# Kernel tuning notes

Measured on AMD Instinct MI355X. Metric: run time of the kernel, lower is better.

Reference implementation:

```python
import jax, jax.numpy as jnp
import numpy as np
from jax import lax

DIM = 512
MED = 2 * DIM            # expansion_ratio * dim
NF = 4                   # num_filters
SIZE = 64                # spatial size (H = W = size)
FS = SIZE // 2 + 1       # rfft filter size
HR = int(0.5 * DIM)      # reweight hidden (NNConv, 1x1 convs)
HS = int(0.5 * DIM)      # spatial_reweight hidden (Convs, 3x3 convs)
B = 16


def _conv1x1(x, w, b):
    # x: [B,C,H,W], w: [O,C,1,1]
    return jnp.einsum('bchw,oc->bohw', x, w[:, :, 0, 0]) + b[None, :, None, None]


def _conv3x3(x, w, b):
    # x: [B,C,H,W], w: [O,C,3,3], padding=1
    return lax.conv_general_dilated(x, w, (1, 1), 'SAME') + b[None, :, None, None]


def setup_inputs() -> dict:
    key = jax.random.key(0)
    ks = jax.random.split(key, 12)
    n = lambda k, shape, s=0.02: jax.random.normal(k, shape, jnp.float32) * s
    return dict(
        x=jax.random.normal(ks[0], (B, DIM, SIZE, SIZE), jnp.float32),
        w_pw1=n(ks[1], (MED, DIM)),                 # pwconv1 (Linear, no bias)
        w_pw2=n(ks[2], (DIM, MED)),                 # pwconv2 (Linear, no bias)
        star_scale=jnp.ones((1,), jnp.float32),     # StarReLU scale
        star_bias=jnp.zeros((1,), jnp.float32),     # StarReLU bias
        rw_fc1_w=n(ks[3], (HR, DIM, 1, 1)), rw_fc1_b=jnp.zeros((HR,), jnp.float32),
        rw_conv_w=n(ks[4], (HR, HR, 1, 1)), rw_conv_b=jnp.zeros((HR,), jnp.float32),
        rw_fc2_w=n(ks[5], (NF * MED, HR, 1, 1)), rw_fc2_b=jnp.zeros((NF * MED,), jnp.float32),
        sp_fc1_w=n(ks[6], (HS, DIM, 3, 3)), sp_fc1_b=jnp.zeros((HS,), jnp.float32),
        sp_fc2_w=n(ks[7], (NF * MED, HS, 3, 3)), sp_fc2_b=jnp.zeros((NF * MED,), jnp.float32),
        complex_weights=n(ks[8], (SIZE, FS, NF, 2), 0.02),
        spatial_weights=n(ks[9], (SIZE, SIZE, NF), 0.03),
    )


def reference(x, w_pw1, w_pw2, star_scale, star_bias,
              rw_fc1_w, rw_fc1_b, rw_conv_w, rw_conv_b, rw_fc2_w, rw_fc2_b,
              sp_fc1_w, sp_fc1_b, sp_fc2_w, sp_fc2_b,
              complex_weights, spatial_weights):
    Bn, _, H, W = x.shape
    # --- routing branch (NNConv: 1x1 conv -> relu -> 1x1 conv -> relu -> 1x1 conv) ---
    r = jax.nn.relu(_conv1x1(x, rw_fc1_w, rw_fc1_b))
    r = jax.nn.relu(_conv1x1(r, rw_conv_w, rw_conv_b))
    r = _conv1x1(r, rw_fc2_w, rw_fc2_b)                      # [B, NF*MED, H, W]
    routeing = jax.nn.softmax(r.mean(axis=(2, 3)).reshape(Bn, NF, MED), axis=1)
    # --- spatial routing branch (Convs: 3x3 conv -> relu -> 3x3 conv) ---
    s = jax.nn.relu(_conv3x3(x, sp_fc1_w, sp_fc1_b))
    s = _conv3x3(s, sp_fc2_w, sp_fc2_b)                      # [B, NF*MED, H, W]
    spatial_routeing = jax.nn.softmax(s.mean(axis=(2, 3)).reshape(Bn, NF, MED), axis=1)
    # --- main path ---
    xc = jnp.transpose(x, (0, 2, 3, 1))                      # [B,H,W,DIM]
    xp = jnp.einsum('bhwc,mc->bhwm', xc, w_pw1)              # pwconv1 -> [B,H,W,MED]
    xp = star_scale * jnp.square(jax.nn.relu(xp)) + star_bias  # StarReLU
    xf = jnp.fft.rfft2(xp, axes=(1, 2), norm='ortho')        # [B,H,FS,MED] complex64
    cw = lax.complex(complex_weights[..., 0], complex_weights[..., 1])  # [H,FS,NF]
    weight = jnp.einsum('bfc,hwf->bhwc', routeing.astype(cw.dtype), cw)  # [B,H,FS,MED]
    spatial_weight = jnp.einsum('bfc,hwf->bhwc', spatial_routeing, spatial_weights)  # [B,H,W,MED]
    xs = jnp.fft.irfft2(xf * weight, s=(H, W), axes=(1, 2), norm='ortho')
    out = xp * spatial_weight + xs                            # spatial gating + FFT filter
    out = jnp.einsum('bhwm,dm->bhwd', out, w_pw2)             # pwconv2
    return jnp.transpose(out, (0, 3, 1, 2))                   # [B,DIM,H,W]
```

## Files before the change

### kernel.cpp

```cpp
#include <hip/hip_runtime.h>

#define HW    4096
#define DIMC  512
#define MEDC  1024
#define HRC   256
#define HSC   256
#define NBATCH 16

typedef __attribute__((ext_vector_type(8))) short bf16x8;
typedef __attribute__((ext_vector_type(4))) float f32x4;

static const size_t R1_OFF    = 0;
static const size_t XT_OFF    = 8388608;
static const size_t WCONV_OFF = 25165824;
static const size_t WR1_OFF   = 25755648;
static const size_t WRC_OFF   = 25821184;
static const size_t XP_OFF    = 0;
static const size_t WB1_OFF   = 67108864;
static const size_t WB2_OFF   = 67371008;
static const size_t MEAN_OFF  = 67633152;
static const size_t AGG_OFF   = MEAN_OFF + 4096;
static const size_t TAP_OFF   = AGG_OFF + 36864;
static const size_t ROUTE_OFF = TAP_OFF + 36864;
static const size_t SR_OFF    = ROUTE_OFF + 65536;
static const size_t WS_END    = SR_OFF + 65536;

__device__ __forceinline__ unsigned short f2bf(float f) {
  unsigned u = __float_as_uint(f);
  unsigned r = (u + 0x7fffu + ((u >> 16) & 1u)) >> 16;
  return (unsigned short)r;
}

__global__ __launch_bounds__(256) void cvt_bf16(
    const float* __restrict__ src, unsigned short* __restrict__ dst, int n)
{
  int i = blockIdx.x * 256 + threadIdx.x;
  if (i < n) dst[i] = f2bf(src[i]);
}

__global__ __launch_bounds__(256) void xpose_bf16(
    const float* __restrict__ x, unsigned short* __restrict__ xT)
{
  __shared__ unsigned short T[32][33];
  const int tid = threadIdx.x;
  const int p0 = blockIdx.x * 32, c0 = blockIdx.y * 32, bb = blockIdx.z;
#pragma unroll
  for (int i = 0; i < 4; i++) {
    int idx = i * 256 + tid;
    int c_l = idx >> 5, p_l = idx & 31;
    T[c_l][p_l] = f2bf(x[((size_t)(bb * DIMC + c0 + c_l)) * HW + p0 + p_l]);
  }
  __syncthreads();
#pragma unroll
  for (int i = 0; i < 4; i++) {
    int idx = i * 256 + tid;
    int p_l = idx >> 5, c_l = idx & 31;
    xT[((size_t)bb * HW + p0 + p_l) * DIMC + c0 + c_l] = T[c_l][p_l];
  }
}

__global__ __launch_bounds__(256) void wconv_bf16(
    const float* __restrict__ w, unsigned short* __restrict__ wbf)
{
  int idx = blockIdx.x * 256 + threadIdx.x;
  if (idx < HSC * DIMC) {
#pragma unroll
    for (int t = 0; t < 9; t++)
      wbf[(size_t)t * (HSC * DIMC) + idx] = f2bf(w[(size_t)idx * 9 + t]);
  }
}

template<int EPI, int ASRC>
__global__ __launch_bounds__(256) void gemm_bf16(
    const void* __restrict__ Aptr, const unsigned short* __restrict__ Wb,
    const float* __restrict__ bias, float* __restrict__ Cf,
    unsigned short* __restrict__ Cb, float* __restrict__ meansum,
    const float* __restrict__ star_scale, const float* __restrict__ star_bias,
    int K, int Ntot)
{
  __shared__ __align__(16) unsigned short As[128 * 40];
  __shared__ __align__(16) unsigned short Bs[128 * 40];
  const int tid = threadIdx.x;
  const int pix0 = blockIdx.x * 128;
  const int n0g = blockIdx.y * 128;
  const int bb = blockIdx.z;
  const int wid = tid >> 6, lane = tid & 63;
  const int lo = lane & 15, hi = lane >> 4;
  const int wm = wid >> 1, wn = wid & 1;

  f32x4 acc[4][4];
#pragma unroll
  for (int mi = 0; mi < 4; mi++)
#pragma unroll
    for (int ni = 0; ni < 4; ni++) acc[mi][ni] = (f32x4){0.f, 0.f, 0.f, 0.f};

  const int nsteps = K >> 5;
  for (int s = 0; s < nsteps; s++) {
    const int c0 = s * 32;
    if (ASRC == 0) {
      const unsigned short* AT = (const unsigned short*)Aptr;
#pragma unroll
      for (int it = 0; it < 2; it++) {
        int idx = it * 256 + tid;
        int p = idx >> 2, co = (idx & 3) * 8;
        uint4 v = *(const uint4*)&AT[((size_t)bb * HW + pix0 + p) * K + c0 + co];
        *(uint4*)&As[p * 40 + co] = v;
      }
    } else {
      const float* Af = (const float*)Aptr;
#pragma unroll
      for (int it = 0; it < 16; it++) {
        int idx = it * 256 + tid;
        int k_l = idx >> 7, p_l = idx & 127;
        float v = Af[((size_t)bb * K + c0 + k_l) * HW + pix0 + p_l];
        As[p_l * 40 + k_l] = f2bf(v);
      }
    }
#pragma unroll
    for (int it = 0; it < 2; it++) {
      int idx = it * 256 + tid;
      int o = idx >> 2, co = (idx & 3) * 8;
      uint4 v = *(const uint4*)&Wb[(size_t)(n0g + o) * K + c0 + co];
      *(uint4*)&Bs[o * 40 + co] = v;
    }
    __syncthreads();

    bf16x8 a[4], bq[4];
#pragma unroll
    for (int mi = 0; mi < 4; mi++)
      a[mi] = *(const bf16x8*)&As[(wm * 64 + mi * 16 + lo) * 40 + hi * 8];
#pragma unroll
    for (int ni = 0; ni < 4; ni++)
      bq[ni] = *(const bf16x8*)&Bs[(wn * 64 + ni * 16 + lo) * 40 + hi * 8];
#pragma unroll
    for (int mi = 0; mi < 4; mi++)
#pragma unroll
      for (int ni = 0; ni < 4; ni++)
        acc[mi][ni] = __builtin_amdgcn_mfma_f32_16x16x32_bf16(a[mi], bq[ni], acc[mi][ni], 0, 0, 0);
    __syncthreads();
  }

  if (EPI == 3) {
#pragma unroll
    for (int ni = 0; ni < 4; ni++) {
      const int n = n0g + wn * 64 + ni * 16 + lo;
      const float bia = bias[n];
      float T = 0.f;
#pragma unroll
      for (int mi = 0; mi < 4; mi++)
#pragma unroll
        for (int r = 0; r < 4; r++)
          T += fmaxf(acc[mi][ni][r] + bia, 0.f);
      T += __shfl_xor(T, 16);
      T += __shfl_xor(T, 32);
      if (hi == 0) atomicAdd(&meansum[bb * Ntot + n], T);
    }
    return;
  }

  if (EPI == 1) {
#pragma unroll
    for (int ni = 0; ni < 4; ni++) {
      const int n = n0g + wn * 64 + ni * 16 + lo;
      const float bia = bias[n];
#pragma unroll
      for (int mi = 0; mi < 4; mi++)
#pragma unroll
        for (int r = 0; r < 4; r++) {
          const int pix = pix0 + wm * 64 + mi * 16 + hi * 4 + r;
          Cb[((size_t)bb * HW + pix) * Ntot + n] = f2bf(fmaxf(acc[mi][ni][r] + bia, 0.f));
        }
    }
    return;
  }

  float ss = 1.f, sb = 0.f;
  if (EPI == 2) { ss = star_scale[0]; sb = star_bias[0]; }
#pragma unroll
  for (int ni = 0; ni < 4; ni++) {
    const int n = n0g + wn * 64 + ni * 16 + lo;
#pragma unroll
    for (int mi = 0; mi < 4; mi++) {
      const int pixb = pix0 + wm * 64 + mi * 16 + hi * 4;
      float4 v;
      float* vv = (float*)&v;
#pragma unroll
      for (int r = 0; r < 4; r++) {
        float t = acc[mi][ni][r];
        if (EPI == 2) { t = fmaxf(t, 0.f); t = ss * t * t + sb; }
        vv[r] = t;
      }
      *(float4*)&Cf[((size_t)bb * Ntot + n) * HW + pixb] = v;
    }
  }
}

__global__ __launch_bounds__(256) void conv3_mfma(
    const unsigned short* __restrict__ xT, const unsigned short* __restrict__ wbf,
    const float* __restrict__ bias, float* __restrict__ agg)
{
  __shared__ __align__(16) unsigned short As[128 * 40];
  __shared__ __align__(16) unsigned short Bs[128 * 40];
  const int tid = threadIdx.x;
  const int bx = blockIdx.x;
  const int n0g = blockIdx.y * 128;
  const int bb = blockIdx.z;
  const int h0 = bx * 2;
  const int wid = tid >> 6;
  const int lane = tid & 63;
  const int lo = lane & 15, hi = lane >> 4;
  const int wm = wid >> 1;
  const int wn = wid & 1;

  f32x4 acc[4][4];
#pragma unroll
  for (int mi = 0; mi < 4; mi++)
#pragma unroll
    for (int ni = 0; ni < 4; ni++) acc[mi][ni] = (f32x4){0.f, 0.f, 0.f, 0.f};

  for (int s = 0; s < 144; s++) {
    const int t = s >> 4;
    const int c0 = (s & 15) * 32;
    const int di = t / 3 - 1, dj = t % 3 - 1;
#pragma unroll
    for (int it = 0; it < 2; it++) {
      int idx = it * 256 + tid;
      int pix = idx >> 2, co = (idx & 3) * 8;
      int h = h0 + (pix >> 6) + di;
      int col = (pix & 63) + dj;
      uint4 v = make_uint4(0u, 0u, 0u, 0u);
      if (h >= 0 && h < 64 && col >= 0 && col < 64)
        v = *(const uint4*)&xT[((size_t)bb * HW + h * 64 + col) * DIMC + c0 + co];
      *(uint4*)&As[pix * 40 + co] = v;
    }
#pragma unroll
    for (int it = 0; it < 2; it++) {
      int idx = it * 256 + tid;
      int o = idx >> 2, co = (idx & 3) * 8;
      uint4 v = *(const uint4*)&wbf[((size_t)t * (HSC * DIMC)) + (size_t)(n0g + o) * DIMC + c0 + co];
      *(uint4*)&Bs[o * 40 + co] = v;
    }
    __syncthreads();

    bf16x8 a[4], bfr[4];
#pragma unroll
    for (int mi = 0; mi < 4; mi++)
      a[mi] = *(const bf16x8*)&As[(wm * 64 + mi * 16 + lo) * 40 + hi * 8];
#pragma unroll
    for (int ni = 0; ni < 4; ni++)
      bfr[ni] = *(const bf16x8*)&Bs[(wn * 64 + ni * 16 + lo) * 40 + hi * 8];
#pragma unroll
    for (int mi = 0; mi < 4; mi++)
#pragma unroll
      for (int ni = 0; ni < 4; ni++)
        acc[mi][ni] = __builtin_amdgcn_mfma_f32_16x16x32_bf16(a[mi], bfr[ni], acc[mi][ni], 0, 0, 0);
    __syncthreads();
  }

  const int h = h0 + wm;
#pragma unroll
  for (int ni = 0; ni < 4; ni++) {
    const int o = n0g + wn * 64 + ni * 16 + lo;
    const float bia = bias[o];
    float T = 0.f;
#pragma unroll
    for (int mi = 0; mi < 4; mi++)
#pragma unroll
      for (int r = 0; r < 4; r++)
        T += fmaxf(acc[mi][ni][r] + bia, 0.f);
    T += __shfl_xor(T, 16);
    T += __shfl_xor(T, 32);
    float* ag = &agg[((size_t)bb * HSC + o) * 9];
    if (hi == 0) {
      atomicAdd(ag + 0, T);
      if (h == 0)  atomicAdd(ag + 1, T);
      if (h == 63) atomicAdd(ag + 2, T);
      float c0v = fmaxf(acc[0][ni][0] + bia, 0.f);
      atomicAdd(ag + 3, c0v);
      if (h == 0)  atomicAdd(ag + 5, c0v);
      if (h == 63) atomicAdd(ag + 7, c0v);
    }
    if (hi == 3) {
      float cwv = fmaxf(acc[3][ni][3] + bia, 0.f);
      atomicAdd(ag + 4, cwv);
      if (h == 0)  atomicAdd(ag + 6, cwv);
      if (h == 63) atomicAdd(ag + 8, cwv);
    }
  }
}

__global__ void tap_compute(const float* __restrict__ agg, float* __restrict__ tap)
{
  int b = blockIdx.x; int c = threadIdx.x;
  const float* a = &agg[((size_t)b * HSC + c) * 9];
  float T = a[0], R0 = a[1], RH = a[2], C0 = a[3], CW = a[4];
  float s00 = a[5], s0W = a[6], sH0 = a[7], sHW = a[8];
  float* tp = &tap[((size_t)b * HSC + c) * 9];
#pragma unroll
  for (int i = 0; i < 3; i++)
#pragma unroll
    for (int j = 0; j < 3; j++) {
      int di = i - 1, dj = j - 1;
      float v = T;
      if (di == -1) v -= RH; else if (di == 1) v -= R0;
      if (dj == -1) v -= CW; else if (dj == 1) v -= C0;
      if (di == -1 && dj == -1) v += sHW;
      if (di == -1 && dj ==  1) v += sH0;
      if (di ==  1 && dj == -1) v += s0W;
      if (di ==  1 && dj ==  1) v += s00;
      tp[i * 3 + j] = v * (1.f / 4096.f);
    }
}

__global__ __launch_bounds__(256) void route_softmax(
    const float* __restrict__ meansum, const float* __restrict__ W,
    const float* __restrict__ bias, float* __restrict__ route)
{
  __shared__ float mv[HRC];
  int b = blockIdx.y;
  int m = blockIdx.x * 256 + threadIdx.x;
  mv[threadIdx.x] = meansum[b * HRC + threadIdx.x] * (1.f / 4096.f);
  __syncthreads();
  float l[4];
#pragma unroll
  for (int f = 0; f < 4; f++) {
    int o = f * MEDC + m;
    float accv = bias[o];
    const float* wr = &W[(size_t)o * HRC];
    for (int c = 0; c < HRC; c++) accv += wr[c] * mv[c];
    l[f] = accv;
  }
  float mx = fmaxf(fmaxf(l[0], l[1]), fmaxf(l[2], l[3]));
  float e[4], s = 0.f;
#pragma unroll
  for (int f = 0; f < 4; f++) { e[f] = expf(l[f] - mx); s += e[f]; }
  float inv = 1.f / s;
#pragma unroll
  for (int f = 0; f < 4; f++) route[((size_t)b * 4 + f) * MEDC + m] = e[f] * inv;
}

__global__ __launch_bounds__(256) void sproute_softmax(
    const float* __restrict__ tap, const float* __restrict__ W,
    const float* __restrict__ bias, float* __restrict__ sroute)
{
  __shared__ float tv[HSC * 9];
  int b = blockIdx.y;
  int m = blockIdx.x * 256 + threadIdx.x;
#pragma unroll
  for (int i = 0; i < 9; i++) {
    int idx = i * 256 + threadIdx.x;
    tv[idx] = tap[(size_t)b * HSC * 9 + idx];
  }
  __syncthreads();
  float l[4];
#pragma unroll
  for (int f = 0; f < 4; f++) {
    int o = f * MEDC + m;
    float accv = bias[o];
    const float* wr = &W[(size_t)o * HSC * 9];
    for (int ct = 0; ct < HSC * 9; ct++) accv += wr[ct] * tv[ct];
    l[f] = accv;
  }
  float mx = fmaxf(fmaxf(l[0], l[1]), fmaxf(l[2], l[3]));
  float e[4], s = 0.f;
#pragma unroll
  for (int f = 0; f < 4; f++) { e[f] = expf(l[f] - mx); s += e[f]; }
  float inv = 1.f / s;
#pragma unroll
  for (int f = 0; f < 4; f++) sroute[((size_t)b * 4 + f) * MEDC + m] = e[f] * inv;
}

constexpr float TWC64[64] = {
  1.00000000f, 0.99518473f, 0.98078528f, 0.95694034f, 0.92387953f, 0.88192126f, 0.83146961f, 0.77301045f,
  0.70710678f, 0.63439328f, 0.55557023f, 0.47139674f, 0.38268343f, 0.29028468f, 0.19509032f, 0.09801714f,
  0.00000000f,-0.09801714f,-0.19509032f,-0.29028468f,-0.38268343f,-0.47139674f,-0.55557023f,-0.63439328f,
 -0.70710678f,-0.77301045f,-0.83146961f,-0.88192126f,-0.92387953f,-0.95694034f,-0.98078528f,-0.99518473f,
 -1.00000000f,-0.99518473f,-0.98078528f,-0.95694034f,-0.92387953f,-0.88192126f,-0.83146961f,-0.77301045f,
 -0.70710678f,-0.63439328f,-0.55557023f,-0.47139674f,-0.38268343f,-0.29028468f,-0.19509032f,-0.09801714f,
 -0.00000000f, 0.09801714f, 0.19509032f, 0.29028468f, 0.38268343f, 0.47139674f, 0.55557023f, 0.63439328f,
  0.70710678f, 0.77301045f, 0.83146961f, 0.88192126f, 0.92387953f, 0.95694034f, 0.98078528f, 0.99518473f
};
constexpr float TWS64[64] = {
  0.00000000f, 0.09801714f, 0.19509032f, 0.29028468f, 0.38268343f, 0.47139674f, 0.55557023f, 0.63439328f,
  0.70710678f, 0.77301045f, 0.83146961f, 0.88192126f, 0.92387953f, 0.95694034f, 0.98078528f, 0.99518473f,
  1.00000000f, 0.99518473f, 0.98078528f, 0.95694034f, 0.92387953f, 0.88192126f, 0.83146961f, 0.77301045f,
  0.70710678f, 0.63439328f, 0.55557023f, 0.47139674f, 0.38268343f, 0.29028468f, 0.19509032f, 0.09801714f,
  0.00000000f,-0.09801714f,-0.19509032f,-0.29028468f,-0.38268343f,-0.47139674f,-0.55557023f,-0.63439328f,
 -0.70710678f,-0.77301045f,-0.83146961f,-0.88192126f,-0.92387953f,-0.95694034f,-0.98078528f,-0.99518473f,
 -1.00000000f,-0.99518473f,-0.98078528f,-0.95694034f,-0.92387953f,-0.88192126f,-0.83146961f,-0.77301045f,
 -0.70710678f,-0.63439328f,-0.55557023f,-0.47139674f,-0.38268343f,-0.29028468f,-0.19509032f,-0.09801714f
};

template<int SGN>
__device__ __forceinline__ void dft8(const float* xr, const float* xi, float* Xr, float* Xi) {
  const float S = (float)SGN;
  const float r = 0.70710678118654752440f;
  float t0r = xr[0] + xr[4], t0i = xi[0] + xi[4];
  float t1r = xr[0] - xr[4], t1i = xi[0] - xi[4];
  float t2r = xr[2] + xr[6], t2i = xi[2] + xi[6];
  float t3r = xr[2] - xr[6], t3i = xi[2] - xi[6];
  float E0r = t0r + t2r, E0i = t0i + t2i;
  float E2r = t0r - t2r, E2i = t0i - t2i;
  float E1r = t1r - S * t3i, E1i = t1i + S * t3r;
  float E3r = t1r + S * t3i, E3i = t1i - S * t3r;
  float u0r = xr[1] + xr[5], u0i = xi[1] + xi[5];
  float u1r = xr[1] - xr[5], u1i = xi[1] - xi[5];
  float u2r = xr[3] + xr[7], u2i = xi[3] + xi[7];
  float u3r = xr[3] - xr[7], u3i = xi[3] - xi[7];
  float O0r = u0r + u2r, O0i = u0i + u2i;
  float O2r = u0r - u2r, O2i = u0i - u2i;
  float O1r = u1r - S * u3i, O1i = u1i + S * u3r;
  float O3r = u1r + S * u3i, O3i = u1i - S * u3r;
  float p1r = r * (O1r - S * O1i), p1i = r * (S * O1r + O1i);
  float p2r = -S * O2i,            p2i = S * O2r;
  float p3r = -r * (O3r + S * O3i), p3i = r * (S * O3r - O3i);
  Xr[0] = E0r + O0r; Xi[0] = E0i + O0i;
  Xr[4] = E0r - O0r; Xi[4] = E0i - O0i;
  Xr[1] = E1r + p1r; Xi[1] = E1i + p1i;
  Xr[5] = E1r - p1r; Xi[5] = E1i - p1i;
  Xr[2] = E2r + p2r; Xi[2] = E2i + p2i;
  Xr[6] = E2r - p2r; Xi[6] = E2i - p2i;
  Xr[3] = E3r + p3r; Xi[3] = E3i + p3i;
  Xr[7] = E3r - p3r; Xi[7] = E3i - p3i;
}

template<int SGN>
__device__ __forceinline__ void dft8_strided(float* xr, float* xi, const int base, const int stride) {
  float ar[8], ai[8], Br[8], Bi[8];
#pragma unroll
  for (int j = 0; j < 8; j++) { ar[j] = xr[base + j * stride]; ai[j] = xi[base + j * stride]; }
  dft8<SGN>(ar, ai, Br, Bi);
#pragma unroll
  for (int j = 0; j < 8; j++) { xr[base + j * stride] = Br[j]; xi[base + j * stride] = Bi[j]; }
}

template<int SGN>
__device__ __forceinline__ void twiddle_all(float* xr, float* xi) {
#pragma unroll
  for (int s = 0; s < 64; s++) {
    const int a = (s >> 3) * (s & 7);
    if (a) {
      const float c = TWC64[a];
      const float si = (float)SGN * TWS64[a];
      float rr = xr[s] * c - xi[s] * si;
      xi[s] = xr[s] * si + xi[s] * c;
      xr[s] = rr;
    }
  }
}

template<int SGN>
__device__ __forceinline__ void fft64_n2r(float* xr, float* xi) {
#pragma unroll
  for (int g = 0; g < 8; g++) dft8_strided<SGN>(xr, xi, g, 8);
  twiddle_all<SGN>(xr, xi);
#pragma unroll
  for (int g = 0; g < 8; g++) dft8_strided<SGN>(xr, xi, 8 * g, 1);
}

template<int SGN>
__device__ __forceinline__ void fft64_r2n(float* xr, float* xi) {
#pragma unroll
  for (int g = 0; g < 8; g++) dft8_strided<SGN>(xr, xi, 8 * g, 1);
  twiddle_all<SGN>(xr, xi);
#pragma unroll
  for (int g = 0; g < 8; g++) dft8_strided<SGN>(xr, xi, g, 8);
}

__global__ __launch_bounds__(128, 1) void fft_filter(
    float* __restrict__ xp, const float* __restrict__ route,
    const float* __restrict__ sroute, const float* __restrict__ cw,
    const float* __restrict__ spw)
{
  __shared__ float Sbuf[2 * 64 * 66];
  const int wave = threadIdx.x >> 6;
  const int lane = threadIdx.x & 63;
  float* S = &Sbuf[wave * (64 * 66)];
  float2* Fs = (float2*)S;
  const int blk = blockIdx.x * 2 + wave;
  const int b = blk >> 10;
  const int m = blk & 1023;
  float* img = xp + (size_t)blk * HW;

  float r4[4], s4[4];
#pragma unroll
  for (int f = 0; f < 4; f++) {
    r4[f] = route[((size_t)b * 4 + f) * MEDC + m] * (1.f / 4096.f);
    s4[f] = sroute[((size_t)b * 4 + f) * MEDC + m];
  }

#pragma unroll
  for (int t = 0; t < 16; t++) {
    const int idx = t * 64 + lane;
    float4 v = *(const float4*)&img[idx * 4];
    const int row = idx >> 4;
    const int col = (idx & 15) * 4;
    S[row * 65 + col + 0] = v.x;
    S[row * 65 + col + 1] = v.y;
    S[row * 65 + col + 2] = v.z;
    S[row * 65 + col + 3] = v.w;
  }
  __syncthreads();

  float xr[64], xi[64];

#pragma unroll
  for (int w = 0; w < 64; w++) { xr[w] = S[lane * 65 + w]; xi[w] = 0.f; }
  __syncthreads();
  fft64_n2r<-1>(xr, xi);
#pragma unroll
  for (int k1 = 0; k1 < 8; k1++)
#pragma unroll
    for (int k2 = 0; k2 < 5; k2++) {
      const int k = k1 + 8 * k2;
      if (k <= 32)
        Fs[lane * 33 + k] = make_float2(xr[8 * k1 + k2], xi[8 * k1 + k2]);
    }
  __syncthreads();

  if (lane < 33) {
#pragma unroll
    for (int h = 0; h < 64; h++) {
      float2 v = Fs[h * 33 + lane];
      xr[h] = v.x; xi[h] = v.y;
    }
    fft64_n2r<-1>(xr, xi);
#pragma unroll
    for (int s = 0; s < 64; s++) {
      const int kh = (s >> 3) + 8 * (s & 7);
      const float* cwp = &cw[(size_t)(kh * 33 + lane) * 8];
      float4 c0 = *(const float4*)cwp;
      float4 c1 = *(const float4*)(cwp + 4);
      float wre = r4[0] * c0.x + r4[1] * c0.z + r4[2] * c1.x + r4[3] * c1.z;
      float wim = r4[0] * c0.y + r4[1] * c0.w + r4[2] * c1.y + r4[3] * c1.w;
      float rr = xr[s] * wre - xi[s] * wim;
      xi[s] = xr[s] * wim + xi[s] * wre;
      xr[s] = rr;
    }
    fft64_r2n<1>(xr, xi);
#pragma unroll
    for (int h = 0; h < 64; h++)
      Fs[h * 33 + lane] = make_float2(xr[h], xi[h]);
  }
  __syncthreads();

#pragma unroll
  for (int k = 0; k < 33; k++) {
    float2 v = Fs[lane * 33 + k];
    if (k == 0 || k == 32) { xr[k] = v.x; xi[k] = 0.f; }
    else                   { xr[k] = 2.f * v.x; xi[k] = 2.f * v.y; }
  }
#pragma unroll
  for (int k = 33; k < 64; k++) { xr[k] = 0.f; xi[k] = 0.f; }
  __syncthreads();

  fft64_n2r<1>(xr, xi);

#pragma unroll
  for (int t = 0; t < 16; t++) {
    const int idx = t * 64 + lane;
    float4 v = *(const float4*)&img[idx * 4];
    const int row = idx >> 4;
    const int col = (idx & 15) * 4;
    S[row * 65 + col + 0] = v.x;
    S[row * 65 + col + 1] = v.y;
    S[row * 65 + col + 2] = v.z;
    S[row * 65 + col + 3] = v.w;
  }
  __syncthreads();

#pragma unroll
  for (int w = 0; w < 64; w++) {
    const int s = 8 * (w & 7) + (w >> 3);
    float4 sp = *(const float4*)&spw[(size_t)(lane * 64 + w) * 4];
    float sw = s4[0] * sp.x + s4[1] * sp.y + s4[2] * sp.z + s4[3] * sp.w;
    S[lane * 65 + w] = S[lane * 65 + w] * sw + xr[s];
  }
  __syncthreads();

#pragma unroll
  for (int t = 0; t < 16; t++) {
    const int idx = t * 64 + lane;
    const int row = idx >> 4;
    const int col = (idx & 15) * 4;
    float4 o;
    o.x = S[row * 65 + col + 0];
    o.y = S[row * 65 + col + 1];
    o.z = S[row * 65 + col + 2];
    o.w = S[row * 65 + col + 3];
    *(float4*)&img[idx * 4] = o;
  }
}

extern "C" void kernel_launch(void* const* d_in, const int* in_sizes, int n_in,
                              void* d_out, int out_size, void* d_ws, size_t ws_size,
                              hipStream_t stream) {
  const float* x          = (const float*)d_in[0];
  const float* w_pw1      = (const float*)d_in[1];
  const float* w_pw2      = (const float*)d_in[2];
  const float* star_scale = (const float*)d_in[3];
  const float* star_bias  = (const float*)d_in[4];
  const float* rw1w = (const float*)d_in[5];
  const float* rw1b = (const float*)d_in[6];
  const float* rwcw = (const float*)d_in[7];
  const float* rwcb = (const float*)d_in[8];
  const float* rw2w = (const float*)d_in[9];
  const float* rw2b = (const float*)d_in[10];
  const float* sp1w = (const float*)d_in[11];
  const float* sp1b = (const float*)d_in[12];
  const float* sp2w = (const float*)d_in[13];
  const float* sp2b = (const float*)d_in[14];
  const float* cw   = (const float*)d_in[15];
  const float* spw  = (const float*)d_in[16];

  if (ws_size < WS_END * sizeof(float)) return;

  float* ws = (float*)d_ws;
  float* xp = ws + XP_OFF;
  unsigned short* r1    = (unsigned short*)(ws + R1_OFF);
  unsigned short* xT    = (unsigned short*)(ws + XT_OFF);
  unsigned short* wconv = (unsigned short*)(ws + WCONV_OFF);
  unsigned short* wr1   = (unsigned short*)(ws + WR1_OFF);
  unsigned short* wrc   = (unsigned short*)(ws + WRC_OFF);
  unsigned short* wb1   = (unsigned short*)(ws + WB1_OFF);
  unsigned short* wb2   = (unsigned short*)(ws + WB2_OFF);
  float* meansum = ws + MEAN_OFF;
  float* agg     = ws + AGG_OFF;
  float* tap     = ws + TAP_OFF;
  float* route   = ws + ROUTE_OFF;
  float* sr      = ws + SR_OFF;
  float* out = (float*)d_out;

  hipMemsetAsync(meansum, 0, (4096 + 36864) * sizeof(float), stream);

  xpose_bf16<<<dim3(128, 16, 16), 256, 0, stream>>>(x, xT);
  wconv_bf16<<<512, 256, 0, stream>>>(sp1w, wconv);
  cvt_bf16<<<2048, 256, 0, stream>>>(w_pw1, wb1, MEDC * DIMC);
  cvt_bf16<<<2048, 256, 0, stream>>>(w_pw2, wb2, DIMC * MEDC);
  cvt_bf16<<<512, 256, 0, stream>>>(rw1w, wr1, HRC * DIMC);
  cvt_bf16<<<256, 256, 0, stream>>>(rwcw, wrc, HRC * HRC);

  gemm_bf16<1, 0><<<dim3(32, 2, 16), 256, 0, stream>>>(
      xT, wr1, rw1b, nullptr, r1, nullptr, nullptr, nullptr, DIMC, HRC);
  gemm_bf16<3, 0><<<dim3(32, 2, 16), 256, 0, stream>>>(
      r1, wrc, rwcb, nullptr, nullptr, meansum, nullptr, nullptr, HRC, HRC);
  route_softmax<<<dim3(4, 16), 256, 0, stream>>>(meansum, rw2w, rw2b, route);

  conv3_mfma<<<dim3(32, 2, 16), 256, 0, stream>>>(xT, wconv, sp1b, agg);
  tap_compute<<<16, 256, 0, stream>>>(agg, tap);
  sproute_softmax<<<dim3(4, 16), 256, 0, stream>>>(tap, sp2w, sp2b, sr);

  gemm_bf16<2, 1><<<dim3(32, 8, 16), 256, 0, stream>>>(
      x, wb1, nullptr, xp, nullptr, nullptr, star_scale, star_bias, DIMC, MEDC);
  fft_filter<<<8192, 128, 0, stream>>>(xp, route, sr, cw, spw);
  gemm_bf16<0, 1><<<dim3(32, 4, 16), 256, 0, stream>>>(
      xp, wb2, nullptr, out, nullptr, nullptr, nullptr, nullptr, MEDC, DIMC);
}
```

Baseline: 1.640 ms.

## Stage halo tile once per channel chunk in 3x3 conv and vectorize fp32 A loads

The 3x3 conv kernel now loads a 4x66 haloed input tile into shared memory once per 32-channel chunk. All nine taps read shifted windows of that tile, instead of each tap reloading 128 pixels from global memory. This cuts input global traffic by about ninefold, at the cost of larger shared memory use. Separately, the fp32-to-bf16 A-operand staging in the GEMM kernel now uses float4 loads instead of scalar loads, which gives fewer but wider global memory transactions.

```diff
diff --git a/kernel.cpp b/kernel.cpp
--- a/kernel.cpp
+++ b/kernel.cpp
@@ -109,11 +109,14 @@
     } else {
       const float* Af = (const float*)Aptr;
 #pragma unroll
-      for (int it = 0; it < 16; it++) {
+      for (int it = 0; it < 4; it++) {
         int idx = it * 256 + tid;
-        int k_l = idx >> 7, p_l = idx & 127;
-        float v = Af[((size_t)bb * K + c0 + k_l) * HW + pix0 + p_l];
-        As[p_l * 40 + k_l] = f2bf(v);
+        int k_l = idx >> 5, p4 = (idx & 31) * 4;
+        float4 v = *(const float4*)&Af[((size_t)bb * K + c0 + k_l) * HW + pix0 + p4];
+        As[(p4 + 0) * 40 + k_l] = f2bf(v.x);
+        As[(p4 + 1) * 40 + k_l] = f2bf(v.y);
+        As[(p4 + 2) * 40 + k_l] = f2bf(v.z);
+        As[(p4 + 3) * 40 + k_l] = f2bf(v.w);
       }
     }
 #pragma unroll
@@ -199,7 +202,7 @@
     const unsigned short* __restrict__ xT, const unsigned short* __restrict__ wbf,
     const float* __restrict__ bias, float* __restrict__ agg)
 {
-  __shared__ __align__(16) unsigned short As[128 * 40];
+  __shared__ __align__(16) unsigned short Xs[4 * 66 * 40];
   __shared__ __align__(16) unsigned short Bs[128 * 40];
   const int tid = threadIdx.x;
   const int bx = blockIdx.x;
@@ -218,43 +221,49 @@
 #pragma unroll
     for (int ni = 0; ni < 4; ni++) acc[mi][ni] = (f32x4){0.f, 0.f, 0.f, 0.f};
 
-  for (int s = 0; s < 144; s++) {
-    const int t = s >> 4;
-    const int c0 = (s & 15) * 32;
-    const int di = t / 3 - 1, dj = t % 3 - 1;
-#pragma unroll
-    for (int it = 0; it < 2; it++) {
+  for (int ch = 0; ch < 16; ch++) {
+    const int c0 = ch * 32;
+#pragma unroll
+    for (int it = 0; it < 5; it++) {
       int idx = it * 256 + tid;
-      int pix = idx >> 2, co = (idx & 3) * 8;
-      int h = h0 + (pix >> 6) + di;
-      int col = (pix & 63) + dj;
-      uint4 v = make_uint4(0u, 0u, 0u, 0u);
-      if (h >= 0 && h < 64 && col >= 0 && col < 64)
-        v = *(const uint4*)&xT[((size_t)bb * HW + h * 64 + col) * DIMC + c0 + co];
-      *(uint4*)&As[pix * 40 + co] = v;
-    }
-#pragma unroll
-    for (int it = 0; it < 2; it++) {
-      int idx = it * 256 + tid;
-      int o = idx >> 2, co = (idx & 3) * 8;
-      uint4 v = *(const uint4*)&wbf[((size_t)t * (HSC * DIMC)) + (size_t)(n0g + o) * DIMC + c0 + co];
-      *(uint4*)&Bs[o * 40 + co] = v;
-    }
-    __syncthreads();
-
-    bf16x8 a[4], bfr[4];
-#pragma unroll
-    for (int mi = 0; mi < 4; mi++)
-      a[mi] = *(const bf16x8*)&As[(wm * 64 + mi * 16 + lo) * 40 + hi * 8];
-#pragma unroll
-    for (int ni = 0; ni < 4; ni++)
-      bfr[ni] = *(const bf16x8*)&Bs[(wn * 64 + ni * 16 + lo) * 40 + hi * 8];
-#pragma unroll
-    for (int mi = 0; mi < 4; mi++)
+      if (idx < 1056) {
+        int pos = idx >> 2, q = idx & 3;
+        int r = pos / 66, cc = pos - r * 66;
+        int h = h0 + r - 1, col = cc - 1;
+        uint4 v = make_uint4(0u, 0u, 0u, 0u);
+        if (h >= 0 && h < 64 && col >= 0 && col < 64)
+          v = *(const uint4*)&xT[((size_t)bb * HW + h * 64 + col) * DIMC + c0 + q * 8];
+        *(uint4*)&Xs[pos * 40 + q * 8] = v;
+      }
+    }
+#pragma unroll
+    for (int t = 0; t < 9; t++) {
+      const int di = t / 3 - 1, dj = t % 3 - 1;
+#pragma unroll
+      for (int it = 0; it < 2; it++) {
+        int idx = it * 256 + tid;
+        int o = idx >> 2, co = (idx & 3) * 8;
+        uint4 v = *(const uint4*)&wbf[((size_t)t * (HSC * DIMC)) + (size_t)(n0g + o) * DIMC + c0 + co];
+        *(uint4*)&Bs[o * 40 + co] = v;
+      }
+      __syncthreads();
+
+      bf16x8 a[4], bfr[4];
+#pragma unroll
+      for (int mi = 0; mi < 4; mi++) {
+        const int col = mi * 16 + lo;
+        a[mi] = *(const bf16x8*)&Xs[((wm + di + 1) * 66 + col + dj + 1) * 40 + hi * 8];
+      }
 #pragma unroll
       for (int ni = 0; ni < 4; ni++)
-        acc[mi][ni] = __builtin_amdgcn_mfma_f32_16x16x32_bf16(a[mi], bfr[ni], acc[mi][ni], 0, 0, 0);
-    __syncthreads();
+        bfr[ni] = *(const bf16x8*)&Bs[(wn * 64 + ni * 16 + lo) * 40 + hi * 8];
+#pragma unroll
+      for (int mi = 0; mi < 4; mi++)
+#pragma unroll
+        for (int ni = 0; ni < 4; ni++)
+          acc[mi][ni] = __builtin_amdgcn_mfma_f32_16x16x32_bf16(a[mi], bfr[ni], acc[mi][ni], 0, 0, 0);
+      __syncthreads();
+    }
   }
 
   const int h = h0 + wm;
```

Result: slower. 1.776 ms (+8.3%).
